# Performance work log

Measured on AMD Instinct MI355X. Metric: run time of the kernel, lower is better.

## Reference

```python
import jax, jax.numpy as jnp
import numpy as np

B, S, H, HEADS = 4, 2048, 512, 8
DK = H // HEADS
LN_EPS = 1e-5
NEG_INF = -1e30


def setup_inputs() -> dict:
    key = jax.random.key(0)
    k = jax.random.split(key, 6)
    x = jax.random.normal(k[0], (B, S, H), dtype=jnp.float32)
    mask = jax.random.randint(k[1], (B, S), 0, 2, dtype=jnp.int32)
    # per-head Q/K/V projection weights stacked: [heads, H, dk]
    Wq = jax.random.normal(k[2], (HEADS, H, DK), dtype=jnp.float32) * 0.05
    Wk = jax.random.normal(k[3], (HEADS, H, DK), dtype=jnp.float32) * 0.05
    Wv = jax.random.normal(k[4], (HEADS, H, DK), dtype=jnp.float32) * 0.05
    # output projection: [heads*dk, H] (y = h @ Wo)
    Wo = jax.random.normal(k[5], (HEADS * DK, H), dtype=jnp.float32) * 0.05
    gamma = jnp.ones((H,), dtype=jnp.float32)
    beta = jnp.zeros((H,), dtype=jnp.float32)
    return {"x": x, "mask": mask, "Wq": Wq, "Wk": Wk, "Wv": Wv,
            "Wo": Wo, "gamma": gamma, "beta": beta}


def reference(x, mask, Wq, Wk, Wv, Wo, gamma, beta):
    # LayerNorm over hidden dim
    mu = jnp.mean(x, axis=-1, keepdims=True)
    var = jnp.mean(jnp.square(x - mu), axis=-1, keepdims=True)
    xn = (x - mu) * jax.lax.rsqrt(var + LN_EPS) * gamma + beta  # [B,S,H]

    mf = mask.astype(jnp.float32)  # [B,S]

    # batched per-head projections (original loops over heads)
    q = jnp.einsum('bsh,nhd->bnsd', xn, Wq)  # [B,heads,S,dk]
    kk = jnp.einsum('bsh,nhd->bnsd', xn, Wk)
    v = jnp.einsum('bsh,nhd->bnsd', xn, Wv)

    scores = jnp.einsum('bnqd,bnkd->bnqk', q, kk) / np.sqrt(DK).astype(np.float32)
    m = mf[:, None, None, :]  # [B,1,1,S] broadcast over query dim
    logits = m * scores + (1.0 - m) * NEG_INF
    probs = jax.nn.softmax(logits, axis=-1)
    attn = jnp.einsum('bnqk,bnkd->bnqd', probs, v)  # [B,heads,S,dk]

    h = attn.transpose(0, 2, 1, 3).reshape(x.shape[0], x.shape[1], HEADS * DK)
    out = h @ Wo + xn          # residual adds post-norm x (as in original)
    out = out * mf[:, :, None]  # zero out masked positions
    return out
```

## Files before the change

kernel.cpp:

```cpp
#include <hip/hip_runtime.h>
#include <hip/hip_bf16.h>
#include <math.h>

#define B_ 4
#define S_ 2048
#define H_ 512
#define HEADS_ 8
#define DK_ 64
#define NROWS_ (B_*S_)
#define LN_EPS_ 1e-5f
#define NEG_INF_ -1e30f
#define QSCALE_ (0.125f * 1.44269504088896f)

typedef short s8v __attribute__((ext_vector_type(8)));
typedef short s4v __attribute__((ext_vector_type(4)));
typedef float f4v __attribute__((ext_vector_type(4)));

typedef __attribute__((address_space(1))) unsigned int gu32_t;
typedef __attribute__((address_space(3))) unsigned int lu32_t;

__device__ __forceinline__ unsigned short f2bf(float f) {
    unsigned int u = __float_as_uint(f);
    u += 0x7FFFu + ((u >> 16) & 1u);
    return (unsigned short)(u >> 16);
}

__device__ __forceinline__ float bf2f(unsigned short u) {
    return __uint_as_float((unsigned int)u << 16);
}

__device__ __forceinline__ s4v pk4bf(float a, float b, float c, float d) {
    union { __hip_bfloat162 h[2]; s4v v; } u;
    u.h[0] = __float22bfloat162_rn(float2{a, b});
    u.h[1] = __float22bfloat162_rn(float2{c, d});
    return u.v;
}

__global__ __launch_bounds__(256) void prep_kernel(
        const float* __restrict__ x, const float* __restrict__ gamma,
        const float* __restrict__ beta, const int* __restrict__ mask,
        const float* __restrict__ Wq, const float* __restrict__ Wk,
        const float* __restrict__ Wv, const float* __restrict__ Wo,
        unsigned short* __restrict__ xnb, float* __restrict__ mb,
        unsigned short* __restrict__ Wt) {
    int bx = blockIdx.x;
    if (bx < 2048) {
        int row  = bx * 4 + (threadIdx.x >> 6);
        int lane = threadIdx.x & 63;
        const float4* xr = (const float4*)(x + (size_t)row * H_ + lane * 8);
        float4 a = xr[0], d = xr[1];
        float s  = (a.x + a.y) + (a.z + a.w) + (d.x + d.y) + (d.z + d.w);
        float ss = (a.x*a.x + a.y*a.y) + (a.z*a.z + a.w*a.w)
                 + (d.x*d.x + d.y*d.y) + (d.z*d.z + d.w*d.w);
        #pragma unroll
        for (int i = 1; i < 64; i <<= 1) {
            s  += __shfl_xor(s, i, 64);
            ss += __shfl_xor(ss, i, 64);
        }
        float mu  = s * (1.f / 512.f);
        float var = ss * (1.f / 512.f) - mu * mu;
        float rstd = rsqrtf(var + LN_EPS_);
        if (lane == 0) mb[row] = mask[row] ? 0.f : NEG_INF_;
        const float4* gp = (const float4*)(gamma + lane * 8);
        const float4* bp = (const float4*)(beta + lane * 8);
        float4 g0 = gp[0], g1 = gp[1], b0 = bp[0], b1 = bp[1];
        float4 y0, y1;
        y0.x = (a.x - mu) * rstd * g0.x + b0.x;
        y0.y = (a.y - mu) * rstd * g0.y + b0.y;
        y0.z = (a.z - mu) * rstd * g0.z + b0.z;
        y0.w = (a.w - mu) * rstd * g0.w + b0.w;
        y1.x = (d.x - mu) * rstd * g1.x + b1.x;
        y1.y = (d.y - mu) * rstd * g1.y + b1.y;
        y1.z = (d.z - mu) * rstd * g1.z + b1.z;
        y1.w = (d.w - mu) * rstd * g1.w + b1.w;
        union { s4v h[2]; s8v v; } pk;
        pk.h[0] = pk4bf(y0.x, y0.y, y0.z, y0.w);
        pk.h[1] = pk4bf(y1.x, y1.y, y1.z, y1.w);
        *(s8v*)(xnb + (size_t)row * H_ + lane * 8) = pk.v;
    } else {
        __shared__ float tile[32][33];
        int wid = bx - 2048;
        const float* src;
        int ld, drow, k0, c0;
        float scale = 1.f;
        if (wid < 768) {
            int z = wid >> 5, rem = wid & 31;
            int cx = rem & 1, ky = rem >> 1;
            k0 = ky * 32; c0 = cx * 32;
            int zw = z >> 3, head = z & 7;
            const float* W = (zw == 0) ? Wq : (zw == 1) ? Wk : Wv;
            if (zw == 0) scale = QSCALE_;
            src = W + (size_t)head * H_ * DK_;
            ld = DK_;
            drow = zw * 512 + head * 64;
        } else {
            int rem = wid - 768;
            int cx = rem & 15, ky = rem >> 4;
            k0 = ky * 32; c0 = cx * 32;
            src = Wo; ld = H_; drow = 1536;
        }
        int tx = threadIdx.x & 31, ty = threadIdx.x >> 5;
        #pragma unroll
        for (int i = 0; i < 4; i++)
            tile[ty * 4 + i][tx] = src[(size_t)(k0 + ty * 4 + i) * ld + c0 + tx];
        __syncthreads();
        #pragma unroll
        for (int i = 0; i < 4; i++) {
            int cc = ty * 4 + i;
            Wt[(size_t)(drow + c0 + cc) * 512 + k0 + tx] = f2bf(tile[tx][cc] * scale);
        }
    }
}

__device__ __forceinline__ void gemm_tile(
        const unsigned short* __restrict__ A,
        const unsigned short* __restrict__ Bt,
        int r0, int j0, f4v acc[4][4]) {
    __shared__ unsigned short As[3 * 128 * 32];
    __shared__ unsigned short Bs[3 * 128 * 32];
    int t = threadIdx.x;
    int wv = t >> 6, L = t & 63, c = L & 15, g = L >> 4;
    int m_base = (wv & 1) * 64, n_base = (wv >> 1) * 64;
    #pragma unroll
    for (int i = 0; i < 4; i++)
        #pragma unroll
        for (int j = 0; j < 4; j++) acc[i][j] = (f4v){0.f, 0.f, 0.f, 0.f};

    auto stage = [&](int buf, int k0) {
        #pragma unroll
        for (int i = 0; i < 2; i++) {
            int uu = wv * 128 + i * 64 + L;
            int row = uu >> 2, k16 = uu & 3;
            __builtin_amdgcn_global_load_lds(
                (const gu32_t*)(A + (size_t)(r0 + row) * 512 + k0 + k16 * 8),
                (lu32_t*)(As + buf * 4096 + (size_t)(wv * 128 + i * 64) * 8), 16, 0, 0);
            __builtin_amdgcn_global_load_lds(
                (const gu32_t*)(Bt + (size_t)(j0 + row) * 512 + k0 + k16 * 8),
                (lu32_t*)(Bs + buf * 4096 + (size_t)(wv * 128 + i * 64) * 8), 16, 0, 0);
        }
    };

    auto compute = [&](int buf) {
        s8v a[4], b[4];
        #pragma unroll
        for (int i = 0; i < 4; i++)
            a[i] = *(const s8v*)(As + buf * 4096 + (size_t)(m_base + i * 16 + c) * 32 + g * 8);
        #pragma unroll
        for (int j = 0; j < 4; j++)
            b[j] = *(const s8v*)(Bs + buf * 4096 + (size_t)(n_base + j * 16 + c) * 32 + g * 8);
        #pragma unroll
        for (int i = 0; i < 4; i++)
            #pragma unroll
            for (int j = 0; j < 4; j++)
                acc[i][j] = __builtin_amdgcn_mfma_f32_16x16x32_bf16(
                    a[i], b[j], acc[i][j], 0, 0, 0);
    };

    stage(0, 0);
    stage(1, 32);
    #pragma unroll
    for (int s = 0; s < 14; ++s) {
        stage((s + 2) % 3, (s + 2) * 32);
        __asm__ volatile("s_waitcnt vmcnt(8)" ::: "memory");
        __builtin_amdgcn_s_barrier();
        compute(s % 3);
        __builtin_amdgcn_s_barrier();
    }
    __asm__ volatile("s_waitcnt vmcnt(4)" ::: "memory");
    __builtin_amdgcn_s_barrier();
    compute(14 % 3);
    __builtin_amdgcn_s_barrier();
    __asm__ volatile("s_waitcnt vmcnt(0)" ::: "memory");
    __builtin_amdgcn_s_barrier();
    compute(15 % 3);
}

__global__ __launch_bounds__(256) void qkv_gemm(
        const unsigned short* __restrict__ xnb,
        const unsigned short* __restrict__ Wt,
        unsigned short* __restrict__ Qb, unsigned short* __restrict__ Kf,
        unsigned short* __restrict__ Vf) {
    f4v acc[4][4];
    int t = threadIdx.x;
    int wv = t >> 6, L = t & 63, c = L & 15, g = L >> 4;
    int rb = wv & 1, cb = wv >> 1;
    if (blockIdx.x < 8) {
        int m0 = blockIdx.x * 128, n0 = blockIdx.y * 128;
        gemm_tile(Wt, xnb, m0, n0, acc);
        int R0 = m0 + rb * 64;
        int C0 = n0 + cb * 64;
        int hd = (R0 >> 6) & 7;
        int b  = C0 >> 11, srow0 = C0 & 2047;
        size_t bhbase = (size_t)(b * HEADS_ + hd) * S_ * DK_;
        if (R0 < 512) {
            #pragma unroll
            for (int msub = 0; msub < 4; msub++) {
                int dk4 = msub * 16 + g * 4;
                #pragma unroll
                for (int nsub = 0; nsub < 4; nsub++) {
                    int tok = srow0 + nsub * 16 + c;
                    s4v v = pk4bf(acc[msub][nsub][0], acc[msub][nsub][1],
                                  acc[msub][nsub][2], acc[msub][nsub][3]);
                    *(s4v*)(Qb + bhbase + (size_t)tok * DK_ + dk4) = v;
                }
            }
        } else {
            unsigned short* dst = Kf + bhbase + (size_t)(srow0 >> 6) * 4096;
            #pragma unroll
            for (int msub = 0; msub < 4; msub++) {
                int gx = (msub & 1) * 2 + (g >> 1);
                int slotbase = (g & 1) * 4 + (msub >> 1) * 8;
                #pragma unroll
                for (int nsub = 0; nsub < 4; nsub++) {
                    s4v v = pk4bf(acc[msub][nsub][0], acc[msub][nsub][1],
                                  acc[msub][nsub][2], acc[msub][nsub][3]);
                    *(s4v*)(dst + nsub * 1024 + (gx * 16 + c) * 16 + slotbase) = v;
                }
            }
        }
    } else {
        int r0 = blockIdx.y * 128, j0 = 1024 + (blockIdx.x - 8) * 128;
        gemm_tile(xnb, Wt, r0, j0, acc);
        int R0 = r0 + rb * 64;
        int C0 = j0 + cb * 64;
        int hd = (C0 >> 6) & 7;
        int b = R0 >> 11, srow0 = R0 & 2047;
        unsigned short* dst = Vf + (size_t)(b * HEADS_ + hd) * S_ * DK_
                              + (size_t)(srow0 >> 6) * 4096;
        #pragma unroll
        for (int msub = 0; msub < 4; msub++)
            #pragma unroll
            for (int nsub = 0; nsub < 4; nsub++) {
                s4v v = pk4bf(acc[msub][nsub][0], acc[msub][nsub][1],
                              acc[msub][nsub][2], acc[msub][nsub][3]);
                *(s4v*)(dst + nsub * 1024 + (g * 16 + c) * 16 + msub * 4) = v;
            }
    }
}

#define LOAD_KVH(pfx, hh) do {                                             \
    int kb_ = (hh) >> 1, h_ = (hh) & 1;                                    \
    const unsigned short* Kn_ = Kp + (size_t)kb_ * 4096;                   \
    const unsigned short* Vn_ = Vp + (size_t)kb_ * 4096;                   \
    pfx##k0lo = *(const s8v*)(Kn_ + (h_ * 2 + 0) * 1024);                  \
    pfx##k0hi = *(const s8v*)(Kn_ + (h_ * 2 + 0) * 1024 + 8);              \
    pfx##k1lo = *(const s8v*)(Kn_ + (h_ * 2 + 1) * 1024);                  \
    pfx##k1hi = *(const s8v*)(Kn_ + (h_ * 2 + 1) * 1024 + 8);              \
    pfx##mb0  = *(const float4*)(mbrow + kb_ * 64 + h_ * 32 + g * 4);      \
    pfx##mb1  = *(const float4*)(mbrow + kb_ * 64 + h_ * 32 + 16 + g * 4); \
    pfx##v0 = *(const s8v*)(Vn_ + 0 * 1024 + h_ * 8);                      \
    pfx##v1 = *(const s8v*)(Vn_ + 1 * 1024 + h_ * 8);                      \
    pfx##v2 = *(const s8v*)(Vn_ + 2 * 1024 + h_ * 8);                      \
    pfx##v3 = *(const s8v*)(Vn_ + 3 * 1024 + h_ * 8);                      \
} while (0)

#define COMPUTE_HALF(pfx) do {                                                   \
    f4v bias0 = (f4v){pfx##mb0.x, pfx##mb0.y, pfx##mb0.z, pfx##mb0.w};           \
    f4v bias1 = (f4v){pfx##mb1.x, pfx##mb1.y, pfx##mb1.z, pfx##mb1.w};           \
    f4v sA0 = bias0, sA1 = bias1, sB0 = bias0, sB1 = bias1;                      \
    __builtin_amdgcn_s_setprio(1);                                               \
    sA0 = __builtin_amdgcn_mfma_f32_16x16x32_bf16(pfx##k0lo, qfA0, sA0, 0, 0, 0);\
    sA0 = __builtin_amdgcn_mfma_f32_16x16x32_bf16(pfx##k0hi, qfA1, sA0, 0, 0, 0);\
    sA1 = __builtin_amdgcn_mfma_f32_16x16x32_bf16(pfx##k1lo, qfA0, sA1, 0, 0, 0);\
    sA1 = __builtin_amdgcn_mfma_f32_16x16x32_bf16(pfx##k1hi, qfA1, sA1, 0, 0, 0);\
    sB0 = __builtin_amdgcn_mfma_f32_16x16x32_bf16(pfx##k0lo, qfB0, sB0, 0, 0, 0);\
    sB0 = __builtin_amdgcn_mfma_f32_16x16x32_bf16(pfx##k0hi, qfB1, sB0, 0, 0, 0);\
    sB1 = __builtin_amdgcn_mfma_f32_16x16x32_bf16(pfx##k1lo, qfB0, sB1, 0, 0, 0);\
    sB1 = __builtin_amdgcn_mfma_f32_16x16x32_bf16(pfx##k1hi, qfB1, sB1, 0, 0, 0);\
    __builtin_amdgcn_s_setprio(0);                                               \
    float pA0[4], pA1[4], pB0[4], pB1[4];                                        \
    _Pragma("unroll")                                                            \
    for (int r = 0; r < 4; r++) {                                                \
        pA0[r] = __builtin_amdgcn_exp2f(sA0[r]);                                 \
        pA1[r] = __builtin_amdgcn_exp2f(sA1[r]);                                 \
        pB0[r] = __builtin_amdgcn_exp2f(sB0[r]);                                 \
        pB1[r] = __builtin_amdgcn_exp2f(sB1[r]);                                 \
        lacA[r] += pA0[r] + pA1[r];                                              \
        lacB[r] += pB0[r] + pB1[r];                                              \
    }                                                                            \
    s4v pfA0 = pk4bf(pA0[0], pA0[1], pA0[2], pA0[3]);                            \
    s4v pfA1 = pk4bf(pA1[0], pA1[1], pA1[2], pA1[3]);                            \
    s4v pfB0 = pk4bf(pB0[0], pB0[1], pB0[2], pB0[3]);                            \
    s4v pfB1 = pk4bf(pB1[0], pB1[1], pB1[2], pB1[3]);                            \
    s8v pfa = __builtin_shufflevector(pfA0, pfA1, 0, 1, 2, 3, 4, 5, 6, 7);       \
    s8v pfb = __builtin_shufflevector(pfB0, pfB1, 0, 1, 2, 3, 4, 5, 6, 7);       \
    __builtin_amdgcn_s_setprio(1);                                               \
    accA[0] = __builtin_amdgcn_mfma_f32_16x16x32_bf16(pfx##v0, pfa, accA[0], 0, 0, 0); \
    accB[0] = __builtin_amdgcn_mfma_f32_16x16x32_bf16(pfx##v0, pfb, accB[0], 0, 0, 0); \
    accA[1] = __builtin_amdgcn_mfma_f32_16x16x32_bf16(pfx##v1, pfa, accA[1], 0, 0, 0); \
    accB[1] = __builtin_amdgcn_mfma_f32_16x16x32_bf16(pfx##v1, pfb, accB[1], 0, 0, 0); \
    accA[2] = __builtin_amdgcn_mfma_f32_16x16x32_bf16(pfx##v2, pfa, accA[2], 0, 0, 0); \
    accB[2] = __builtin_amdgcn_mfma_f32_16x16x32_bf16(pfx##v2, pfb, accB[2], 0, 0, 0); \
    accA[3] = __builtin_amdgcn_mfma_f32_16x16x32_bf16(pfx##v3, pfa, accA[3], 0, 0, 0); \
    accB[3] = __builtin_amdgcn_mfma_f32_16x16x32_bf16(pfx##v3, pfb, accB[3], 0, 0, 0); \
    __builtin_amdgcn_s_setprio(0);                                               \
} while (0)

__global__ __launch_bounds__(256, 2) void attn_kernel(
        const unsigned short* __restrict__ Qb,
        const unsigned short* __restrict__ Kf,
        const unsigned short* __restrict__ Vf,
        const float* __restrict__ mb,
        unsigned short* __restrict__ hb) {
    __shared__ float red[2][64][2][17];

    int wv   = threadIdx.x >> 6;
    int qsub = wv & 1;
    int kp   = wv >> 1;
    int L  = threadIdx.x & 63;
    int c  = L & 15;
    int g  = L >> 4;

    unsigned wgid = blockIdx.x + blockIdx.y * 32u;
    unsigned xcd  = wgid & 7u;
    unsigned idx  = wgid >> 3;
    int bh = (int)(xcd + (idx >> 5) * 8u);
    int qt = (int)(idx & 31u);
    int b  = bh >> 3, n = bh & 7;
    int q0 = qt * 64 + qsub * 32;

    const unsigned short* Qbase = Qb + (size_t)bh * S_ * DK_;
    const unsigned short* Kp = Kf + (size_t)bh * S_ * DK_ + (size_t)kp * 16 * 4096 + L * 16;
    const unsigned short* Vp = Vf + (size_t)bh * S_ * DK_ + (size_t)kp * 16 * 4096 + L * 16;
    const float* mbrow = mb + b * S_ + kp * 1024;

    s8v qfA0 = *(const s8v*)(Qbase + (size_t)(q0 + c) * DK_ + g * 8);
    s8v qfA1 = *(const s8v*)(Qbase + (size_t)(q0 + c) * DK_ + 32 + g * 8);
    s8v qfB0 = *(const s8v*)(Qbase + (size_t)(q0 + 16 + c) * DK_ + g * 8);
    s8v qfB1 = *(const s8v*)(Qbase + (size_t)(q0 + 16 + c) * DK_ + 32 + g * 8);

    f4v accA[4], accB[4];
    #pragma unroll
    for (int i = 0; i < 4; i++) {
        accA[i] = (f4v){0.f, 0.f, 0.f, 0.f};
        accB[i] = (f4v){0.f, 0.f, 0.f, 0.f};
    }
    float lacA[4] = {0.f, 0.f, 0.f, 0.f};
    float lacB[4] = {0.f, 0.f, 0.f, 0.f};

    s8v a_k0lo, a_k0hi, a_k1lo, a_k1hi, a_v0, a_v1, a_v2, a_v3;
    float4 a_mb0, a_mb1;
    s8v b_k0lo, b_k0hi, b_k1lo, b_k1hi, b_v0, b_v1, b_v2, b_v3;
    float4 b_mb0, b_mb1;

    LOAD_KVH(a_, 0);
    for (int hh = 0; hh < 32; hh += 2) {
        LOAD_KVH(b_, hh + 1);
        COMPUTE_HALF(a_);
        if (hh + 2 < 32) LOAD_KVH(a_, hh + 2);
        COMPUTE_HALF(b_);
    }

    float lA = (lacA[0] + lacA[1]) + (lacA[2] + lacA[3]);
    float lB = (lacB[0] + lacB[1]) + (lacB[2] + lacB[3]);
    lA += __shfl_xor(lA, 16, 64);
    lA += __shfl_xor(lA, 32, 64);
    lB += __shfl_xor(lB, 16, 64);
    lB += __shfl_xor(lB, 32, 64);

    if (kp == 1) {
        #pragma unroll
        for (int d = 0; d < 4; d++) {
            #pragma unroll
            for (int r = 0; r < 4; r++) {
                red[qsub][L][0][d * 4 + r] = accA[d][r];
                red[qsub][L][1][d * 4 + r] = accB[d][r];
            }
        }
        red[qsub][L][0][16] = lA;
        red[qsub][L][1][16] = lB;
    }
    __syncthreads();
    if (kp == 0) {
        const float* srcA = &red[qsub][L][0][0];
        const float* srcB = &red[qsub][L][1][0];
        float invA = 1.f / (lA + srcA[16]);
        float invB = 1.f / (lB + srcB[16]);
        unsigned short* hpA = hb + (size_t)(b * S_ + q0 + c) * H_ + n * DK_ + g * 4;
        unsigned short* hpB = hpA + (size_t)16 * H_;
        #pragma unroll
        for (int ds = 0; ds < 4; ds++) {
            s4v oA = pk4bf((accA[ds][0] + srcA[ds * 4 + 0]) * invA,
                           (accA[ds][1] + srcA[ds * 4 + 1]) * invA,
                           (accA[ds][2] + srcA[ds * 4 + 2]) * invA,
                           (accA[ds][3] + srcA[ds * 4 + 3]) * invA);
            *(s4v*)(hpA + ds * 16) = oA;
            s4v oB = pk4bf((accB[ds][0] + srcB[ds * 4 + 0]) * invB,
                           (accB[ds][1] + srcB[ds * 4 + 1]) * invB,
                           (accB[ds][2] + srcB[ds * 4 + 2]) * invB,
                           (accB[ds][3] + srcB[ds * 4 + 3]) * invB);
            *(s4v*)(hpB + ds * 16) = oB;
        }
    }
}

__global__ __launch_bounds__(256) void out_gemm(
        const unsigned short* __restrict__ hb,
        const unsigned short* __restrict__ Wot,
        const unsigned short* __restrict__ xnb, const int* __restrict__ mask,
        float* __restrict__ out) {
    f4v acc[4][4];
    int r0 = blockIdx.y * 128, j0 = blockIdx.x * 128;
    gemm_tile(hb, Wot, r0, j0, acc);
    int t = threadIdx.x;
    int wv = t >> 6, L = t & 63, c = L & 15, g = L >> 4;
    int mrow = r0 + (wv & 1) * 64 + g * 4;
    int ncol = j0 + (wv >> 1) * 64 + c;
    #pragma unroll
    for (int msub = 0; msub < 4; msub++) {
        #pragma unroll
        for (int rr = 0; rr < 4; rr++) {
            int row = mrow + msub * 16 + rr;
            float mf = (float)mask[row];
            #pragma unroll
            for (int nsub = 0; nsub < 4; nsub++) {
                int col = ncol + nsub * 16;
                size_t o = (size_t)row * H_ + col;
                out[o] = (acc[msub][nsub][rr] + bf2f(xnb[o])) * mf;
            }
        }
    }
}

extern "C" void kernel_launch(void* const* d_in, const int* in_sizes, int n_in,
                              void* d_out, int out_size, void* d_ws, size_t ws_size,
                              hipStream_t stream) {
    const float* x     = (const float*)d_in[0];
    const int*   mask  = (const int*)d_in[1];
    const float* Wq    = (const float*)d_in[2];
    const float* Wk    = (const float*)d_in[3];
    const float* Wv    = (const float*)d_in[4];
    const float* Wo    = (const float*)d_in[5];
    const float* gamma = (const float*)d_in[6];
    const float* beta  = (const float*)d_in[7];
    float* out = (float*)d_out;

    size_t nelem = (size_t)NROWS_ * H_;
    char* ws = (char*)d_ws;
    unsigned short* xnb = (unsigned short*)ws; ws += nelem * 2;
    unsigned short* hb  = (unsigned short*)ws; ws += nelem * 2;
    unsigned short* Qb  = (unsigned short*)ws; ws += nelem * 2;
    unsigned short* Kf  = (unsigned short*)ws; ws += nelem * 2;
    unsigned short* Vf  = (unsigned short*)ws; ws += nelem * 2;
    unsigned short* Wt  = (unsigned short*)ws; ws += (size_t)2048 * 512 * 2;
    float*          mbp = (float*)ws;

    prep_kernel<<<3072, 256, 0, stream>>>(
        x, gamma, beta, mask, Wq, Wk, Wv, Wo, xnb, mbp, Wt);
    qkv_gemm<<<dim3(12, 64), 256, 0, stream>>>(xnb, Wt, Qb, Kf, Vf);
    attn_kernel<<<dim3(S_ / 64, B_ * HEADS_), 256, 0, stream>>>(
        Qb, Kf, Vf, mbp, hb);
    out_gemm<<<dim3(4, 64), 256, 0, stream>>>(
        hb, Wt + (size_t)1536 * 512, xnb, mask, out);
}
```

Before: 173.3 us.

## Give each attention wave all 64 queries and split keys four ways

```diff
diff --git a/kernel.cpp b/kernel.cpp
--- a/kernel.cpp
+++ b/kernel.cpp
@@ -258,6 +258,7 @@
     f4v bias0 = (f4v){pfx##mb0.x, pfx##mb0.y, pfx##mb0.z, pfx##mb0.w};           \
     f4v bias1 = (f4v){pfx##mb1.x, pfx##mb1.y, pfx##mb1.z, pfx##mb1.w};           \
     f4v sA0 = bias0, sA1 = bias1, sB0 = bias0, sB1 = bias1;                      \
+    f4v sC0 = bias0, sC1 = bias1, sD0 = bias0, sD1 = bias1;                      \
     __builtin_amdgcn_s_setprio(1);                                               \
     sA0 = __builtin_amdgcn_mfma_f32_16x16x32_bf16(pfx##k0lo, qfA0, sA0, 0, 0, 0);\
     sA0 = __builtin_amdgcn_mfma_f32_16x16x32_bf16(pfx##k0hi, qfA1, sA0, 0, 0, 0);\
@@ -267,32 +268,60 @@
     sB0 = __builtin_amdgcn_mfma_f32_16x16x32_bf16(pfx##k0hi, qfB1, sB0, 0, 0, 0);\
     sB1 = __builtin_amdgcn_mfma_f32_16x16x32_bf16(pfx##k1lo, qfB0, sB1, 0, 0, 0);\
     sB1 = __builtin_amdgcn_mfma_f32_16x16x32_bf16(pfx##k1hi, qfB1, sB1, 0, 0, 0);\
+    sC0 = __builtin_amdgcn_mfma_f32_16x16x32_bf16(pfx##k0lo, qfC0, sC0, 0, 0, 0);\
+    sC0 = __builtin_amdgcn_mfma_f32_16x16x32_bf16(pfx##k0hi, qfC1, sC0, 0, 0, 0);\
+    sC1 = __builtin_amdgcn_mfma_f32_16x16x32_bf16(pfx##k1lo, qfC0, sC1, 0, 0, 0);\
+    sC1 = __builtin_amdgcn_mfma_f32_16x16x32_bf16(pfx##k1hi, qfC1, sC1, 0, 0, 0);\
+    sD0 = __builtin_amdgcn_mfma_f32_16x16x32_bf16(pfx##k0lo, qfD0, sD0, 0, 0, 0);\
+    sD0 = __builtin_amdgcn_mfma_f32_16x16x32_bf16(pfx##k0hi, qfD1, sD0, 0, 0, 0);\
+    sD1 = __builtin_amdgcn_mfma_f32_16x16x32_bf16(pfx##k1lo, qfD0, sD1, 0, 0, 0);\
+    sD1 = __builtin_amdgcn_mfma_f32_16x16x32_bf16(pfx##k1hi, qfD1, sD1, 0, 0, 0);\
     __builtin_amdgcn_s_setprio(0);                                               \
-    float pA0[4], pA1[4], pB0[4], pB1[4];                                        \
+    float pA0[4], pA1[4], pB0[4], pB1[4], pC0[4], pC1[4], pD0[4], pD1[4];        \
     _Pragma("unroll")                                                            \
     for (int r = 0; r < 4; r++) {                                                \
         pA0[r] = __builtin_amdgcn_exp2f(sA0[r]);                                 \
         pA1[r] = __builtin_amdgcn_exp2f(sA1[r]);                                 \
         pB0[r] = __builtin_amdgcn_exp2f(sB0[r]);                                 \
         pB1[r] = __builtin_amdgcn_exp2f(sB1[r]);                                 \
+        pC0[r] = __builtin_amdgcn_exp2f(sC0[r]);                                 \
+        pC1[r] = __builtin_amdgcn_exp2f(sC1[r]);                                 \
+        pD0[r] = __builtin_amdgcn_exp2f(sD0[r]);                                 \
+        pD1[r] = __builtin_amdgcn_exp2f(sD1[r]);                                 \
         lacA[r] += pA0[r] + pA1[r];                                              \
         lacB[r] += pB0[r] + pB1[r];                                              \
+        lacC[r] += pC0[r] + pC1[r];                                              \
+        lacD[r] += pD0[r] + pD1[r];                                              \
     }                                                                            \
-    s4v pfA0 = pk4bf(pA0[0], pA0[1], pA0[2], pA0[3]);                            \
-    s4v pfA1 = pk4bf(pA1[0], pA1[1], pA1[2], pA1[3]);                            \
-    s4v pfB0 = pk4bf(pB0[0], pB0[1], pB0[2], pB0[3]);                            \
-    s4v pfB1 = pk4bf(pB1[0], pB1[1], pB1[2], pB1[3]);                            \
-    s8v pfa = __builtin_shufflevector(pfA0, pfA1, 0, 1, 2, 3, 4, 5, 6, 7);       \
-    s8v pfb = __builtin_shufflevector(pfB0, pfB1, 0, 1, 2, 3, 4, 5, 6, 7);       \
+    s8v pfa = __builtin_shufflevector(pk4bf(pA0[0], pA0[1], pA0[2], pA0[3]),     \
+                                      pk4bf(pA1[0], pA1[1], pA1[2], pA1[3]),     \
+                                      0, 1, 2, 3, 4, 5, 6, 7);                   \
+    s8v pfb = __builtin_shufflevector(pk4bf(pB0[0], pB0[1], pB0[2], pB0[3]),     \
+                                      pk4bf(pB1[0], pB1[1], pB1[2], pB1[3]),     \
+                                      0, 1, 2, 3, 4, 5, 6, 7);                   \
+    s8v pfc = __builtin_shufflevector(pk4bf(pC0[0], pC0[1], pC0[2], pC0[3]),     \
+                                      pk4bf(pC1[0], pC1[1], pC1[2], pC1[3]),     \
+                                      0, 1, 2, 3, 4, 5, 6, 7);                   \
+    s8v pfd = __builtin_shufflevector(pk4bf(pD0[0], pD0[1], pD0[2], pD0[3]),     \
+                                      pk4bf(pD1[0], pD1[1], pD1[2], pD1[3]),     \
+                                      0, 1, 2, 3, 4, 5, 6, 7);                   \
     __builtin_amdgcn_s_setprio(1);                                               \
     accA[0] = __builtin_amdgcn_mfma_f32_16x16x32_bf16(pfx##v0, pfa, accA[0], 0, 0, 0); \
     accB[0] = __builtin_amdgcn_mfma_f32_16x16x32_bf16(pfx##v0, pfb, accB[0], 0, 0, 0); \
+    accC[0] = __builtin_amdgcn_mfma_f32_16x16x32_bf16(pfx##v0, pfc, accC[0], 0, 0, 0); \
+    accD[0] = __builtin_amdgcn_mfma_f32_16x16x32_bf16(pfx##v0, pfd, accD[0], 0, 0, 0); \
     accA[1] = __builtin_amdgcn_mfma_f32_16x16x32_bf16(pfx##v1, pfa, accA[1], 0, 0, 0); \
     accB[1] = __builtin_amdgcn_mfma_f32_16x16x32_bf16(pfx##v1, pfb, accB[1], 0, 0, 0); \
+    accC[1] = __builtin_amdgcn_mfma_f32_16x16x32_bf16(pfx##v1, pfc, accC[1], 0, 0, 0); \
+    accD[1] = __builtin_amdgcn_mfma_f32_16x16x32_bf16(pfx##v1, pfd, accD[1], 0, 0, 0); \
     accA[2] = __builtin_amdgcn_mfma_f32_16x16x32_bf16(pfx##v2, pfa, accA[2], 0, 0, 0); \
     accB[2] = __builtin_amdgcn_mfma_f32_16x16x32_bf16(pfx##v2, pfb, accB[2], 0, 0, 0); \
+    accC[2] = __builtin_amdgcn_mfma_f32_16x16x32_bf16(pfx##v2, pfc, accC[2], 0, 0, 0); \
+    accD[2] = __builtin_amdgcn_mfma_f32_16x16x32_bf16(pfx##v2, pfd, accD[2], 0, 0, 0); \
     accA[3] = __builtin_amdgcn_mfma_f32_16x16x32_bf16(pfx##v3, pfa, accA[3], 0, 0, 0); \
     accB[3] = __builtin_amdgcn_mfma_f32_16x16x32_bf16(pfx##v3, pfb, accB[3], 0, 0, 0); \
+    accC[3] = __builtin_amdgcn_mfma_f32_16x16x32_bf16(pfx##v3, pfc, accC[3], 0, 0, 0); \
+    accD[3] = __builtin_amdgcn_mfma_f32_16x16x32_bf16(pfx##v3, pfd, accD[3], 0, 0, 0); \
     __builtin_amdgcn_s_setprio(0);                                               \
 } while (0)
 
@@ -302,11 +331,9 @@
         const unsigned short* __restrict__ Vf,
         const float* __restrict__ mb,
         unsigned short* __restrict__ hb) {
-    __shared__ float red[2][64][2][17];
-
-    int wv   = threadIdx.x >> 6;
-    int qsub = wv & 1;
-    int kp   = wv >> 1;
+    __shared__ float red[3][64][69];
+
+    int kp = threadIdx.x >> 6;
     int L  = threadIdx.x & 63;
     int c  = L & 15;
     int g  = L >> 4;
@@ -317,26 +344,34 @@
     int bh = (int)(xcd + (idx >> 5) * 8u);
     int qt = (int)(idx & 31u);
     int b  = bh >> 3, n = bh & 7;
-    int q0 = qt * 64 + qsub * 32;
+    int q0 = qt * 64;
 
     const unsigned short* Qbase = Qb + (size_t)bh * S_ * DK_;
-    const unsigned short* Kp = Kf + (size_t)bh * S_ * DK_ + (size_t)kp * 16 * 4096 + L * 16;
-    const unsigned short* Vp = Vf + (size_t)bh * S_ * DK_ + (size_t)kp * 16 * 4096 + L * 16;
-    const float* mbrow = mb + b * S_ + kp * 1024;
+    const unsigned short* Kp = Kf + (size_t)bh * S_ * DK_ + (size_t)kp * 8 * 4096 + L * 16;
+    const unsigned short* Vp = Vf + (size_t)bh * S_ * DK_ + (size_t)kp * 8 * 4096 + L * 16;
+    const float* mbrow = mb + b * S_ + kp * 512;
 
     s8v qfA0 = *(const s8v*)(Qbase + (size_t)(q0 + c) * DK_ + g * 8);
     s8v qfA1 = *(const s8v*)(Qbase + (size_t)(q0 + c) * DK_ + 32 + g * 8);
     s8v qfB0 = *(const s8v*)(Qbase + (size_t)(q0 + 16 + c) * DK_ + g * 8);
     s8v qfB1 = *(const s8v*)(Qbase + (size_t)(q0 + 16 + c) * DK_ + 32 + g * 8);
-
-    f4v accA[4], accB[4];
+    s8v qfC0 = *(const s8v*)(Qbase + (size_t)(q0 + 32 + c) * DK_ + g * 8);
+    s8v qfC1 = *(const s8v*)(Qbase + (size_t)(q0 + 32 + c) * DK_ + 32 + g * 8);
+    s8v qfD0 = *(const s8v*)(Qbase + (size_t)(q0 + 48 + c) * DK_ + g * 8);
+    s8v qfD1 = *(const s8v*)(Qbase + (size_t)(q0 + 48 + c) * DK_ + 32 + g * 8);
+
+    f4v accA[4], accB[4], accC[4], accD[4];
     #pragma unroll
     for (int i = 0; i < 4; i++) {
         accA[i] = (f4v){0.f, 0.f, 0.f, 0.f};
         accB[i] = (f4v){0.f, 0.f, 0.f, 0.f};
+        accC[i] = (f4v){0.f, 0.f, 0.f, 0.f};
+        accD[i] = (f4v){0.f, 0.f, 0.f, 0.f};
     }
     float lacA[4] = {0.f, 0.f, 0.f, 0.f};
     float lacB[4] = {0.f, 0.f, 0.f, 0.f};
+    float lacC[4] = {0.f, 0.f, 0.f, 0.f};
+    float lacD[4] = {0.f, 0.f, 0.f, 0.f};
 
     s8v a_k0lo, a_k0hi, a_k1lo, a_k1hi, a_v0, a_v1, a_v2, a_v3;
     float4 a_mb0, a_mb1;
@@ -344,52 +379,79 @@
     float4 b_mb0, b_mb1;
 
     LOAD_KVH(a_, 0);
-    for (int hh = 0; hh < 32; hh += 2) {
+    for (int hh = 0; hh < 16; hh += 2) {
         LOAD_KVH(b_, hh + 1);
         COMPUTE_HALF(a_);
-        if (hh + 2 < 32) LOAD_KVH(a_, hh + 2);
+        if (hh + 2 < 16) LOAD_KVH(a_, hh + 2);
         COMPUTE_HALF(b_);
     }
 
     float lA = (lacA[0] + lacA[1]) + (lacA[2] + lacA[3]);
     float lB = (lacB[0] + lacB[1]) + (lacB[2] + lacB[3]);
+    float lC = (lacC[0] + lacC[1]) + (lacC[2] + lacC[3]);
+    float lD = (lacD[0] + lacD[1]) + (lacD[2] + lacD[3]);
     lA += __shfl_xor(lA, 16, 64);
     lA += __shfl_xor(lA, 32, 64);
     lB += __shfl_xor(lB, 16, 64);
     lB += __shfl_xor(lB, 32, 64);
-
-    if (kp == 1) {
+    lC += __shfl_xor(lC, 16, 64);
+    lC += __shfl_xor(lC, 32, 64);
+    lD += __shfl_xor(lD, 16, 64);
+    lD += __shfl_xor(lD, 32, 64);
+
+    if (kp >= 1) {
+        float* dst = &red[kp - 1][L][0];
         #pragma unroll
         for (int d = 0; d < 4; d++) {
             #pragma unroll
             for (int r = 0; r < 4; r++) {
-                red[qsub][L][0][d * 4 + r] = accA[d][r];
-                red[qsub][L][1][d * 4 + r] = accB[d][r];
+                dst[0 * 17 + d * 4 + r] = accA[d][r];
+                dst[1 * 17 + d * 4 + r] = accB[d][r];
+                dst[2 * 17 + d * 4 + r] = accC[d][r];
+                dst[3 * 17 + d * 4 + r] = accD[d][r];
             }
         }
-        red[qsub][L][0][16] = lA;
-        red[qsub][L][1][16] = lB;
+        dst[0 * 17 + 16] = lA;
+        dst[1 * 17 + 16] = lB;
+        dst[2 * 17 + 16] = lC;
+        dst[3 * 17 + 16] = lD;
     }
     __syncthreads();
     if (kp == 0) {
-        const float* srcA = &red[qsub][L][0][0];
-        const float* srcB = &red[qsub][L][1][0];
-        float invA = 1.f / (lA + srcA[16]);
-        float invB = 1.f / (lB + srcB[16]);
+        #pragma unroll
+        for (int w = 0; w < 3; w++) {
+            const float* s = &red[w][L][0];
+            #pragma unroll
+            for (int d = 0; d < 4; d++) {
+                #pragma unroll
+                for (int r = 0; r < 4; r++) {
+                    accA[d][r] += s[0 * 17 + d * 4 + r];
+                    accB[d][r] += s[1 * 17 + d * 4 + r];
+                    accC[d][r] += s[2 * 17 + d * 4 + r];
+                    accD[d][r] += s[3 * 17 + d * 4 + r];
+                }
+            }
+            lA += s[0 * 17 + 16];
+            lB += s[1 * 17 + 16];
+            lC += s[2 * 17 + 16];
+            lD += s[3 * 17 + 16];
+        }
+        float invA = 1.f / lA, invB = 1.f / lB;
+        float invC = 1.f / lC, invD = 1.f / lD;
         unsigned short* hpA = hb + (size_t)(b * S_ + q0 + c) * H_ + n * DK_ + g * 4;
         unsigned short* hpB = hpA + (size_t)16 * H_;
+        unsigned short* hpC = hpA + (size_t)32 * H_;
+        unsigned short* hpD = hpA + (size_t)48 * H_;
         #pragma unroll
         for (int ds = 0; ds < 4; ds++) {
-            s4v oA = pk4bf((accA[ds][0] + srcA[ds * 4 + 0]) * invA,
-                           (accA[ds][1] + srcA[ds * 4 + 1]) * invA,
-                           (accA[ds][2] + srcA[ds * 4 + 2]) * invA,
-                           (accA[ds][3] + srcA[ds * 4 + 3]) * invA);
-            *(s4v*)(hpA + ds * 16) = oA;
-            s4v oB = pk4bf((accB[ds][0] + srcB[ds * 4 + 0]) * invB,
-                           (accB[ds][1] + srcB[ds * 4 + 1]) * invB,
-                           (accB[ds][2] + srcB[ds * 4 + 2]) * invB,
-                           (accB[ds][3] + srcB[ds * 4 + 3]) * invB);
-            *(s4v*)(hpB + ds * 16) = oB;
+            *(s4v*)(hpA + ds * 16) = pk4bf(accA[ds][0] * invA, accA[ds][1] * invA,
+                                           accA[ds][2] * invA, accA[ds][3] * invA);
+            *(s4v*)(hpB + ds * 16) = pk4bf(accB[ds][0] * invB, accB[ds][1] * invB,
+                                           accB[ds][2] * invB, accB[ds][3] * invB);
+            *(s4v*)(hpC + ds * 16) = pk4bf(accC[ds][0] * invC, accC[ds][1] * invC,
+                                           accC[ds][2] * invC, accC[ds][3] * invC);
+            *(s4v*)(hpD + ds * 16) = pk4bf(accD[ds][0] * invD, accD[ds][1] * invD,
+                                           accD[ds][2] * invD, accD[ds][3] * invD);
         }
     }
 }
```

After: 206.4 us. 19.1% more time.
